# Kernel optimization log

Measured on AMD Instinct MI355X. Metric: run time of the kernel, lower is better.

The kernel has to match this reference:

```python
import jax, jax.numpy as jnp
import numpy as np

N_VERTICES = 50000
N_RADIAL = 5
N_ANGULAR = 8
FEATURE_DIM = 64
AMT_TEMPLATES = 64
TEMPLATE_RADIUS = 0.03
ROTATION_DELTA = 1


def create_template_matrix(n_radial, n_angular, radius):
    # Polar grid of template vertices in cartesian coordinates: (R, A, 2)
    radii = radius * (np.arange(1, n_radial + 1) / n_radial)
    angles = 2.0 * np.pi * np.arange(n_angular) / n_angular
    x = radii[:, None] * np.cos(angles)[None, :]
    y = radii[:, None] * np.sin(angles)[None, :]
    return np.stack([x, y], axis=-1).astype(np.float32)


def define_interpolation_coefficients(template_matrix):
    # Gaussian interpolation prior (concrete instance of the abstract method),
    # normalized over all template vertices. Shape: (R, A, R, A)
    R, A, _ = template_matrix.shape
    flat = template_matrix.reshape(R * A, 2)
    d2 = ((flat[:, None, :] - flat[None, :, :]) ** 2).sum(-1)  # (RA, RA)
    sigma = TEMPLATE_RADIUS / N_RADIAL
    w = np.exp(-d2 / (2.0 * sigma ** 2))
    w = w / w.sum(axis=1, keepdims=True)
    return w.reshape(R, A, R, A).astype(np.float32)


def setup_inputs() -> dict:
    key = jax.random.key(0)
    k1, k2, k3, k4, k5, k6, k7 = jax.random.split(key, 7)
    mesh_signal = jax.random.normal(k1, (N_VERTICES, FEATURE_DIM), dtype=jnp.float32)
    # barycentric coordinates: [..., 0] = vertex index (stored as float),
    # [..., 1] = barycentric weight summing to 1 over the 3 triangle corners
    idx = jax.random.randint(k2, (N_VERTICES, N_RADIAL, N_ANGULAR, 3), 0, N_VERTICES)
    w = jax.random.uniform(k3, (N_VERTICES, N_RADIAL, N_ANGULAR, 3), dtype=jnp.float32)
    w = w / jnp.sum(w, axis=-1, keepdims=True)
    bary_coordinates = jnp.stack([idx.astype(jnp.float32), w], axis=-1)
    neighbor_weights = jax.random.normal(
        k4, (AMT_TEMPLATES, N_RADIAL, N_ANGULAR, FEATURE_DIM), dtype=jnp.float32) * 0.05
    center_weights = jax.random.normal(
        k5, (AMT_TEMPLATES, 1, FEATURE_DIM), dtype=jnp.float32) * 0.05
    bias = jax.random.normal(k6, (AMT_TEMPLATES,), dtype=jnp.float32) * 0.05
    tmpl = create_template_matrix(N_RADIAL, N_ANGULAR, TEMPLATE_RADIUS)
    interp_coeff = jnp.asarray(
        define_interpolation_coefficients(tmpl).reshape(N_RADIAL, N_ANGULAR, N_RADIAL * N_ANGULAR))
    return {
        "mesh_signal": mesh_signal,
        "bary_coordinates": bary_coordinates,
        "neighbor_weights": neighbor_weights,
        "center_weights": center_weights,
        "bias": bias,
        "interp_coeff": interp_coeff,
    }


def reference(mesh_signal, bary_coordinates, neighbor_weights, center_weights, bias, interp_coeff):
    N, R, A, _, _ = bary_coordinates.shape
    C = mesh_signal.shape[-1]
    T = neighbor_weights.shape[0]

    # ---- patch operator: barycentric gather + interpolation ----
    idx = bary_coordinates[..., 0].astype(jnp.int32)          # (N, R, A, 3)
    bw = bary_coordinates[..., 1]                              # (N, R, A, 3)
    gathered = mesh_signal[idx]                                # (N, R, A, 3, C)
    interp = jnp.sum(bw[..., None] * gathered, axis=-2)        # (N, R, A, C)

    # ---- prior: matvec with interpolation coefficients ----
    # original: (N,1,1,C,RA) matvec (R,A,RA) -> (N,R,A,C)
    ms = interp.reshape(N, R * A, C)                           # (N, RA, C)
    interp = jnp.einsum('nmc,ram->nrac', ms, interp_coeff)     # (N, R, A, C)

    # ---- center fold: einsum('si,tji->sjt') ----
    conv_center = jnp.einsum('nc,tjc->njt', mesh_signal, center_weights)  # (N, 1, T)

    # ---- neighbor fold over rotations ----
    # roll(interp, shift=r, axis=angular) . W == interp . roll(W, shift=-r, axis=angular)
    rotations = np.arange(0, A, ROTATION_DELTA)
    w_rot = jnp.stack([jnp.roll(neighbor_weights, -int(r), axis=2) for r in rotations])  # (O, T, R, A, C)
    conv_neighbor = jnp.einsum('nrac,otrac->not', interp, w_rot) + bias                  # (N, O, T)

    return jax.nn.relu(conv_center + conv_neighbor)
```

## Files before the change

### kernel.cpp

```cpp
#include <hip/hip_runtime.h>
#include <hip/hip_bf16.h>

#define N_V   50000
#define CDIM  64
#define RAORD 40
#define KTOT  2624
#define NOUT  512
#define NKB   41
#define BM    128
#define BN    256

typedef short v8s __attribute__((ext_vector_type(8)));
typedef float v4f __attribute__((ext_vector_type(4)));
typedef unsigned short u16;

#define LSTR 72

__device__ __forceinline__ u16 f2bf(float f) {
    unsigned u = __float_as_uint(f);
    return (u16)((u + 0x7FFFu + ((u >> 16) & 1u)) >> 16);
}
__device__ __forceinline__ float bf2f(short s) {
    return __uint_as_float(((unsigned)(unsigned short)s) << 16);
}

__global__ void cast_ms(const float* __restrict__ ms, u16* __restrict__ msb) {
    int i = (blockIdx.x * 256 + threadIdx.x) * 4;
    float4 v = *reinterpret_cast<const float4*>(ms + i);
    ushort4 o;
    o.x = f2bf(v.x); o.y = f2bf(v.y); o.z = f2bf(v.z); o.w = f2bf(v.w);
    *reinterpret_cast<ushort4*>(msb + i) = o;
}

__global__ void build_w2(const float* __restrict__ nw, const float* __restrict__ cw,
                         const float* __restrict__ coeff, u16* __restrict__ w2) {
    __shared__ float scoef[1600];
    __shared__ float snw[2560];
    int j = blockIdx.x;
    int o = j >> 6, t = j & 63;
    int tid = threadIdx.x;
    for (int l = tid; l < 1600; l += 256) scoef[l] = coeff[l];
    for (int l = tid; l < 2560; l += 256) {
        int ra = l >> 6, c = l & 63;
        int r = ra >> 3, a = ra & 7;
        snw[l] = nw[((t * 5 + r) * 8 + ((a + o) & 7)) * 64 + c];
    }
    __syncthreads();
    for (int l = tid; l < 2560; l += 256) {
        int m = l >> 6, c = l & 63;
        float s = 0.f;
        #pragma unroll
        for (int ra = 0; ra < 40; ++ra)
            s += scoef[ra * 40 + m] * snw[ra * 64 + c];
        w2[(size_t)j * KTOT + l] = f2bf(s);
    }
    if (tid < 64) w2[(size_t)j * KTOT + 2560 + tid] = f2bf(cw[t * 64 + tid]);
}

__global__ __launch_bounds__(512, 4)
void gemm_fused(const float* __restrict__ bary, const u16* __restrict__ msb,
                const u16* __restrict__ w2, const float* __restrict__ bias,
                float* __restrict__ out) {
    __shared__ u16 At[BM * LSTR];
    __shared__ u16 Bt[BN * LSTR];

    int tid  = threadIdx.x;
    int lane = tid & 63, wave = tid >> 6;
    int l15  = lane & 15, q = lane >> 4;
    int wm   = wave >> 2, wn = wave & 3;
    int row0 = blockIdx.x * BM;
    int col0 = blockIdx.y * BN;

    v4f acc[4][4];
    #pragma unroll
    for (int mi = 0; mi < 4; ++mi)
        #pragma unroll
        for (int ni = 0; ni < 4; ++ni)
            acc[mi][ni] = (v4f){0.f, 0.f, 0.f, 0.f};

    int ar = tid >> 2;
    int ac = (tid & 3) * 16;
    int an = row0 + ar; if (an > N_V - 1) an = N_V - 1;
    const float* bbase = bary + (size_t)an * 240;

    int bj = tid >> 1;
    int bc = (tid & 1) * 32;
    const u16* wrow = w2 + (size_t)(col0 + bj) * KTOT + bc;

    for (int kb = 0; kb < NKB; ++kb) {
        __syncthreads();

        {
            const u16* src = wrow + kb * 64;
            u16* dst = &Bt[bj * LSTR + bc];
            #pragma unroll
            for (int qq = 0; qq < 4; ++qq)
                *reinterpret_cast<v8s*>(dst + qq * 8) =
                    *reinterpret_cast<const v8s*>(src + qq * 8);
        }

        u16* adst = &At[ar * LSTR + ac];
        if (kb < RAORD) {
            const float* bb = bbase + kb * 6;
            int  i0 = (int)bb[0]; float w0 = bb[1];
            int  i1 = (int)bb[2]; float w1 = bb[3];
            int  i2 = (int)bb[4]; float w2w = bb[5];
            const u16* g0 = msb + (size_t)i0 * 64 + ac;
            const u16* g1 = msb + (size_t)i1 * 64 + ac;
            const u16* g2 = msb + (size_t)i2 * 64 + ac;
            #pragma unroll
            for (int h = 0; h < 2; ++h) {
                v8s a0 = *reinterpret_cast<const v8s*>(g0 + h * 8);
                v8s a1 = *reinterpret_cast<const v8s*>(g1 + h * 8);
                v8s a2 = *reinterpret_cast<const v8s*>(g2 + h * 8);
                v8s r;
                #pragma unroll
                for (int e = 0; e < 8; ++e) {
                    float f = w0 * bf2f(a0[e]) + w1 * bf2f(a1[e]) + w2w * bf2f(a2[e]);
                    r[e] = (short)f2bf(f);
                }
                *reinterpret_cast<v8s*>(adst + h * 8) = r;
            }
        } else {
            const u16* src = msb + (size_t)an * 64 + ac;
            *reinterpret_cast<v8s*>(adst)     = *reinterpret_cast<const v8s*>(src);
            *reinterpret_cast<v8s*>(adst + 8) = *reinterpret_cast<const v8s*>(src + 8);
        }
        __syncthreads();

        #pragma unroll
        for (int s = 0; s < 2; ++s) {
            v8s af[4], bfv[4];
            #pragma unroll
            for (int mi = 0; mi < 4; ++mi)
                af[mi] = *reinterpret_cast<const v8s*>(
                    &At[(wm * 64 + mi * 16 + l15) * LSTR + s * 32 + q * 8]);
            #pragma unroll
            for (int ni = 0; ni < 4; ++ni)
                bfv[ni] = *reinterpret_cast<const v8s*>(
                    &Bt[(wn * 64 + ni * 16 + l15) * LSTR + s * 32 + q * 8]);
            #pragma unroll
            for (int mi = 0; mi < 4; ++mi)
                #pragma unroll
                for (int ni = 0; ni < 4; ++ni)
                    acc[mi][ni] = __builtin_amdgcn_mfma_f32_16x16x32_bf16(
                        af[mi], bfv[ni], acc[mi][ni], 0, 0, 0);
        }
    }

    float bv[4];
    #pragma unroll
    for (int ni = 0; ni < 4; ++ni) bv[ni] = bias[ni * 16 + l15];
    #pragma unroll
    for (int mi = 0; mi < 4; ++mi) {
        int rbase = row0 + wm * 64 + mi * 16 + q * 4;
        #pragma unroll
        for (int ni = 0; ni < 4; ++ni) {
            int cg = col0 + wn * 64 + ni * 16 + l15;
            #pragma unroll
            for (int rg = 0; rg < 4; ++rg) {
                int rr = rbase + rg;
                if (rr < N_V) {
                    float v = acc[mi][ni][rg] + bv[ni];
                    out[(size_t)rr * NOUT + cg] = v > 0.f ? v : 0.f;
                }
            }
        }
    }
}

extern "C" void kernel_launch(void* const* d_in, const int* in_sizes, int n_in,
                              void* d_out, int out_size, void* d_ws, size_t ws_size,
                              hipStream_t stream) {
    const float* ms    = (const float*)d_in[0];
    const float* bary  = (const float*)d_in[1];
    const float* nw    = (const float*)d_in[2];
    const float* cw    = (const float*)d_in[3];
    const float* bias  = (const float*)d_in[4];
    const float* coeff = (const float*)d_in[5];
    float* out = (float*)d_out;

    u16* msb = (u16*)d_ws;
    u16* w2  = (u16*)((char*)d_ws + 6400000);

    cast_ms<<<3125, 256, 0, stream>>>(ms, msb);
    build_w2<<<512, 256, 0, stream>>>(nw, cw, coeff, w2);
    dim3 grid((N_V + BM - 1) / BM, NOUT / BN);
    gemm_fused<<<grid, 512, 0, stream>>>(bary, msb, w2, bias, out);
}
```

Measured before the change: 495.9 us.

## Software-pipeline gather and direct-to-LDS B loads with swizzled LDS in fused GEMM

Rewrites the main GEMM loop as a software pipeline. The bary gathers for the next k-block are prefetched into registers, and the weight tiles are double-buffered through global_load_lds straight into LDS. Hand-placed waitcnt and barrier instructions replace the two __syncthreads per iteration. Padded LDS rows give way to an XOR-swizzled layout, and the interpolation uses packed bf16 arithmetic with perm-based rounding. build_w2 becomes one output element per thread across many blocks, and the grid is linearised. The hand-counted vmcnt values are fragile, and the bf16 rounding is a simplified round-half-up.

```diff
diff --git a/kernel.cpp b/kernel.cpp
--- a/kernel.cpp
+++ b/kernel.cpp
@@ -2,8 +2,6 @@
 #include <hip/hip_bf16.h>
 
 #define N_V   50000
-#define CDIM  64
-#define RAORD 40
 #define KTOT  2624
 #define NOUT  512
 #define NKB   41
@@ -12,16 +10,13 @@
 
 typedef short v8s __attribute__((ext_vector_type(8)));
 typedef float v4f __attribute__((ext_vector_type(4)));
+typedef unsigned int v4u __attribute__((ext_vector_type(4)));
 typedef unsigned short u16;
-
-#define LSTR 72
+typedef unsigned int u32;
 
 __device__ __forceinline__ u16 f2bf(float f) {
-    unsigned u = __float_as_uint(f);
+    u32 u = __float_as_uint(f);
     return (u16)((u + 0x7FFFu + ((u >> 16) & 1u)) >> 16);
-}
-__device__ __forceinline__ float bf2f(short s) {
-    return __uint_as_float(((unsigned)(unsigned short)s) << 16);
 }
 
 __global__ void cast_ms(const float* __restrict__ ms, u16* __restrict__ msb) {
@@ -34,42 +29,64 @@
 
 __global__ void build_w2(const float* __restrict__ nw, const float* __restrict__ cw,
                          const float* __restrict__ coeff, u16* __restrict__ w2) {
-    __shared__ float scoef[1600];
-    __shared__ float snw[2560];
-    int j = blockIdx.x;
+    int l = blockIdx.x * 256 + threadIdx.x;
+    if (l >= NOUT * KTOT) return;
+    int j = l / KTOT, k = l - j * KTOT;
     int o = j >> 6, t = j & 63;
-    int tid = threadIdx.x;
-    for (int l = tid; l < 1600; l += 256) scoef[l] = coeff[l];
-    for (int l = tid; l < 2560; l += 256) {
-        int ra = l >> 6, c = l & 63;
-        int r = ra >> 3, a = ra & 7;
-        snw[l] = nw[((t * 5 + r) * 8 + ((a + o) & 7)) * 64 + c];
+    u16 v;
+    if (k >= 2560) {
+        v = f2bf(cw[t * 64 + (k - 2560)]);
+    } else {
+        int m = k >> 6, c = k & 63;
+        float s = 0.f;
+        #pragma unroll
+        for (int ra = 0; ra < 40; ++ra) {
+            int r = ra >> 3, a = ra & 7;
+            s += coeff[ra * 40 + m] * nw[((t * 5 + r) * 8 + ((a + o) & 7)) * 64 + c];
+        }
+        v = f2bf(s);
     }
-    __syncthreads();
-    for (int l = tid; l < 2560; l += 256) {
-        int m = l >> 6, c = l & 63;
-        float s = 0.f;
-        #pragma unroll
-        for (int ra = 0; ra < 40; ++ra)
-            s += scoef[ra * 40 + m] * snw[ra * 64 + c];
-        w2[(size_t)j * KTOT + l] = f2bf(s);
-    }
-    if (tid < 64) w2[(size_t)j * KTOT + 2560 + tid] = f2bf(cw[t * 64 + tid]);
+    w2[l] = v;
+}
+
+__device__ __forceinline__ void gl2lds(const u16* g, u16* l) {
+    __builtin_amdgcn_global_load_lds(
+        (const __attribute__((address_space(1))) u32*)(uintptr_t)g,
+        (__attribute__((address_space(3))) u32*)(uintptr_t)l, 16, 0, 0);
 }
 
 __global__ __launch_bounds__(512, 4)
 void gemm_fused(const float* __restrict__ bary, const u16* __restrict__ msb,
                 const u16* __restrict__ w2, const float* __restrict__ bias,
                 float* __restrict__ out) {
-    __shared__ u16 At[BM * LSTR];
-    __shared__ u16 Bt[BN * LSTR];
-
-    int tid  = threadIdx.x;
-    int lane = tid & 63, wave = tid >> 6;
-    int l15  = lane & 15, q = lane >> 4;
-    int wm   = wave >> 2, wn = wave & 3;
-    int row0 = blockIdx.x * BM;
-    int col0 = blockIdx.y * BN;
+    __shared__ u16 At[BM * 64];
+    __shared__ u16 Bt[2 * BN * 64];
+
+    const int tid  = threadIdx.x;
+    const int lane = tid & 63, wave = tid >> 6;
+    const int l15  = lane & 15, q = lane >> 4;
+    const int wm   = wave >> 2, wn = wave & 3;
+
+    const int id  = blockIdx.x;
+    const int bx  = id % 391, by = id / 391;
+    const int row0 = bx * BM, col0 = by * BN;
+
+    const int ar  = tid >> 2;
+    const u32 acb = (u32)(tid & 3) * 32;
+    int an = row0 + ar; if (an > N_V - 1) an = N_V - 1;
+    const u32* brow = (const u32*)bary + (size_t)an * 240;
+    const u32 an_off = (u32)an * 128 + acb;
+
+    const int e_a = ar & 7;
+    const u32 at_w0 = (u32)ar * 128 + (u32)(((2 * (tid & 3)) ^ e_a) * 16);
+    const u32 at_w1 = at_w0 ^ 16;
+
+    const int eq = l15 & 7;
+    const u32 a_rd0 = (u32)(wm * 64 + l15) * 128 + (u32)((q ^ eq) * 16);
+    const u32 b_rd0 = (u32)(wn * 64 + l15) * 128 + (u32)((q ^ eq) * 16);
+
+    const int rl = lane >> 3;
+    const int bl = (lane & 7) ^ rl;
 
     v4f acc[4][4];
     #pragma unroll
@@ -78,74 +95,104 @@
         for (int ni = 0; ni < 4; ++ni)
             acc[mi][ni] = (v4f){0.f, 0.f, 0.f, 0.f};
 
-    int ar = tid >> 2;
-    int ac = (tid & 3) * 16;
-    int an = row0 + ar; if (an > N_V - 1) an = N_V - 1;
-    const float* bbase = bary + (size_t)an * 240;
-
-    int bj = tid >> 1;
-    int bc = (tid & 1) * 32;
-    const u16* wrow = w2 + (size_t)(col0 + bj) * KTOT + bc;
-
-    for (int kb = 0; kb < NKB; ++kb) {
-        __syncthreads();
-
-        {
-            const u16* src = wrow + kb * 64;
-            u16* dst = &Bt[bj * LSTR + bc];
-            #pragma unroll
-            for (int qq = 0; qq < 4; ++qq)
-                *reinterpret_cast<v8s*>(dst + qq * 8) =
-                    *reinterpret_cast<const v8s*>(src + qq * 8);
-        }
-
-        u16* adst = &At[ar * LSTR + ac];
-        if (kb < RAORD) {
-            const float* bb = bbase + kb * 6;
-            int  i0 = (int)bb[0]; float w0 = bb[1];
-            int  i1 = (int)bb[2]; float w1 = bb[3];
-            int  i2 = (int)bb[4]; float w2w = bb[5];
-            const u16* g0 = msb + (size_t)i0 * 64 + ac;
-            const u16* g1 = msb + (size_t)i1 * 64 + ac;
-            const u16* g2 = msb + (size_t)i2 * 64 + ac;
-            #pragma unroll
-            for (int h = 0; h < 2; ++h) {
-                v8s a0 = *reinterpret_cast<const v8s*>(g0 + h * 8);
-                v8s a1 = *reinterpret_cast<const v8s*>(g1 + h * 8);
-                v8s a2 = *reinterpret_cast<const v8s*>(g2 + h * 8);
-                v8s r;
-                #pragma unroll
-                for (int e = 0; e < 8; ++e) {
-                    float f = w0 * bf2f(a0[e]) + w1 * bf2f(a1[e]) + w2w * bf2f(a2[e]);
-                    r[e] = (short)f2bf(f);
-                }
-                *reinterpret_cast<v8s*>(adst + h * 8) = r;
-            }
-        } else {
-            const u16* src = msb + (size_t)an * 64 + ac;
-            *reinterpret_cast<v8s*>(adst)     = *reinterpret_cast<const v8s*>(src);
-            *reinterpret_cast<v8s*>(adst + 8) = *reinterpret_cast<const v8s*>(src + 8);
-        }
-        __syncthreads();
-
+    v4u g0a, g0b, g1a, g1b, g2a, g2b;
+    v4u blo, bhi;
+    float w0c, w1c, w2c;
+
+    auto issue_gathers = [&](u32 o0, u32 o1, u32 o2) {
+        const char* mb = (const char*)msb;
+        g0a = *(const v4u*)(mb + o0); g0b = *(const v4u*)(mb + o0 + 16);
+        g1a = *(const v4u*)(mb + o1); g1b = *(const v4u*)(mb + o1 + 16);
+        g2a = *(const v4u*)(mb + o2); g2b = *(const v4u*)(mb + o2 + 16);
+    };
+    auto bary_load = [&](int kc) {
+        u32 d0 = ((u32)(kc * 6)) & ~3u;
+        blo = *(const v4u*)(brow + d0);
+        bhi = *(const v4u*)(brow + d0 + 4);
+    };
+    auto decode_issue = [&](int kc) {
+        u32 uf0, uw0, uf1, uw1, uf2, uw2;
+        if (kc & 1) { uf0 = blo[2]; uw0 = blo[3]; uf1 = bhi[0]; uw1 = bhi[1]; uf2 = bhi[2]; uw2 = bhi[3]; }
+        else        { uf0 = blo[0]; uw0 = blo[1]; uf1 = blo[2]; uw1 = blo[3]; uf2 = bhi[0]; uw2 = bhi[1]; }
+        u32 o0 = ((u32)(int)__uint_as_float(uf0) << 7) + acb;
+        u32 o1 = ((u32)(int)__uint_as_float(uf1) << 7) + acb;
+        u32 o2 = ((u32)(int)__uint_as_float(uf2) << 7) + acb;
+        issue_gathers(o0, o1, o2);
+        w0c = __uint_as_float(uw0); w1c = __uint_as_float(uw1); w2c = __uint_as_float(uw2);
+    };
+    auto ipair = [&](u32 pa, u32 pb, u32 pc) -> u32 {
+        float a0 = __uint_as_float(pa << 16), a1 = __uint_as_float(pa & 0xffff0000u);
+        float b0 = __uint_as_float(pb << 16), b1 = __uint_as_float(pb & 0xffff0000u);
+        float c0 = __uint_as_float(pc << 16), c1 = __uint_as_float(pc & 0xffff0000u);
+        float r0 = w0c * a0 + w1c * b0 + w2c * c0;
+        float r1 = w0c * a1 + w1c * b1 + w2c * c1;
+        return __builtin_amdgcn_perm(__float_as_uint(r1) + 0x8000u,
+                                     __float_as_uint(r0) + 0x8000u, 0x07060302u);
+    };
+    auto blds = [&](int kb_ld, int buf) {
+        #pragma unroll
+        for (int i = 0; i < 4; ++i) {
+            int w_eff = wave * 4 + i;
+            u32 src = (u32)(col0 + w_eff * 8 + rl) * KTOT + (u32)kb_ld * 64 + (u32)(bl * 8);
+            gl2lds(w2 + src, &Bt[buf * (BN * 64) + w_eff * 512]);
+        }
+    };
+    auto mfma_step = [&](int buf) {
+        const char* atp = (const char*)At;
+        const char* btp = (const char*)Bt + buf * (BN * 64 * 2);
         #pragma unroll
         for (int s = 0; s < 2; ++s) {
-            v8s af[4], bfv[4];
-            #pragma unroll
-            for (int mi = 0; mi < 4; ++mi)
-                af[mi] = *reinterpret_cast<const v8s*>(
-                    &At[(wm * 64 + mi * 16 + l15) * LSTR + s * 32 + q * 8]);
-            #pragma unroll
-            for (int ni = 0; ni < 4; ++ni)
-                bfv[ni] = *reinterpret_cast<const v8s*>(
-                    &Bt[(wn * 64 + ni * 16 + l15) * LSTR + s * 32 + q * 8]);
+            u32 ao = a_rd0 ^ (u32)(s * 64), bo = b_rd0 ^ (u32)(s * 64);
+            v8s a_f[4], b_f[4];
+            #pragma unroll
+            for (int mi = 0; mi < 4; ++mi) a_f[mi] = *(const v8s*)(atp + ao + mi * 2048);
+            #pragma unroll
+            for (int ni = 0; ni < 4; ++ni) b_f[ni] = *(const v8s*)(btp + bo + ni * 2048);
             #pragma unroll
             for (int mi = 0; mi < 4; ++mi)
                 #pragma unroll
                 for (int ni = 0; ni < 4; ++ni)
                     acc[mi][ni] = __builtin_amdgcn_mfma_f32_16x16x32_bf16(
-                        af[mi], bfv[ni], acc[mi][ni], 0, 0, 0);
-        }
+                        a_f[mi], b_f[ni], acc[mi][ni], 0, 0, 0);
+        }
+    };
+
+    bary_load(0);
+    decode_issue(0);
+    bary_load(1);
+    blds(0, 0);
+
+    v4u cv0, cv1;
+    #pragma unroll 1
+    for (int kb = 0; kb < NKB; ++kb) {
+        if (kb < 40) {
+            #pragma unroll
+            for (int j = 0; j < 4; ++j) {
+                cv0[j] = ipair(g0a[j], g1a[j], g2a[j]);
+                cv1[j] = ipair(g0b[j], g1b[j], g2b[j]);
+            }
+        } else { cv0 = (v4u)g0a; cv1 = (v4u)g0b; }
+
+        if (kb <= 37)      { decode_issue(kb + 1); bary_load(kb + 2); }
+        else if (kb == 38) { decode_issue(39); }
+        else if (kb == 39) {
+            g0a = *(const v4u*)((const char*)msb + an_off);
+            g0b = *(const v4u*)((const char*)msb + an_off + 16);
+        }
+
+        asm volatile("s_barrier" ::: "memory");
+
+        if (kb <= 39) blds(kb + 1, (kb + 1) & 1);
+
+        *(v4u*)((char*)At + at_w0) = cv0;
+        *(v4u*)((char*)At + at_w1) = cv1;
+
+        if (kb <= 37)      asm volatile("s_waitcnt vmcnt(12) lgkmcnt(0)\ns_barrier" ::: "memory");
+        else if (kb == 38) asm volatile("s_waitcnt vmcnt(10) lgkmcnt(0)\ns_barrier" ::: "memory");
+        else if (kb == 39) asm volatile("s_waitcnt vmcnt(6) lgkmcnt(0)\ns_barrier" ::: "memory");
+        else               asm volatile("s_waitcnt vmcnt(0) lgkmcnt(0)\ns_barrier" ::: "memory");
+
+        mfma_step(kb & 1);
     }
 
     float bv[4];
@@ -184,7 +231,6 @@
     u16* w2  = (u16*)((char*)d_ws + 6400000);
 
     cast_ms<<<3125, 256, 0, stream>>>(ms, msb);
-    build_w2<<<512, 256, 0, stream>>>(nw, cw, coeff, w2);
-    dim3 grid((N_V + BM - 1) / BM, NOUT / BN);
-    gemm_fused<<<grid, 512, 0, stream>>>(bary, msb, w2, bias, out);
-}
+    build_w2<<<(NOUT * KTOT + 255) / 256, 256, 0, stream>>>(nw, cw, coeff, w2);
+    gemm_fused<<<782, 512, 0, stream>>>(bary, msb, w2, bias, out);
+}
```

Measured after the change: 679.0 us. 1.37x slower.
